# Optimization experiments

Hardware: AMD Instinct MI355X
Metric: run time of the kernel (lower is better)

## Reference

```python
import jax, jax.numpy as jnp
import numpy as np

TOP_K = 2
NUM_EXPERTS = 64


def setup_inputs() -> dict:
    key = jax.random.key(0)
    k1, k2 = jax.random.split(key)
    bs, sq, h = 4, 4096, 4096
    x = jax.random.normal(k1, (bs, sq, h), dtype=jnp.float32)
    expert_mask = jnp.ones((bs, NUM_EXPERTS), dtype=jnp.float32)
    # router weight: torch.nn.Linear(hidden, num_experts, bias=False) -> [E, H]
    W = jax.random.normal(k2, (NUM_EXPERTS, h), dtype=jnp.float32) * 0.02
    return {"x": x, "expert_mask": expert_mask, "W": W}


def reference(x, expert_mask, W):
    bs, sq, h = x.shape
    # logits = Linear(x.view(-1, h)) : [bs*sq, E]
    logits = jnp.einsum("bsh,eh->bse", x, W).reshape(bs * sq, NUM_EXPERTS)
    scores = jax.nn.softmax(logits, axis=-1)
    # expert_mask [bs, E] broadcast over seq
    scores = (expert_mask[:, None, :] * scores.reshape(bs, sq, NUM_EXPERTS)).reshape(
        bs * sq, NUM_EXPERTS
    )
    expert_weights, expert_indices = jax.lax.top_k(scores, TOP_K)  # [bs*sq, k]
    expert_weights = jax.nn.softmax(expert_weights, axis=-1)
    # moe_normalize_expert_weights = 1 -> L1 norm renormalization
    expert_weights = expert_weights / jnp.sum(
        jnp.abs(expert_weights), axis=-1, keepdims=True
    )
    return scores, logits, expert_weights, expert_indices
```

## Files before the change

kernel.cpp:

```cpp
#include <hip/hip_runtime.h>
#include <hip/hip_bf16.h>

#define NE     64
#define HDIM   4096
#define NTOK   16384
#define KSPLIT 8
#define KPER   (HDIM / KSPLIT)
#define KC     32
#define NT     (KPER / KC)
#define NCHUNK (HDIM / 32)
#define TOKB   128
#define PT     130

typedef __attribute__((ext_vector_type(8))) short bf16x8;
typedef __attribute__((ext_vector_type(4))) float f32x4;

union FragU { uint4 u; bf16x8 v; };

__device__ __forceinline__ unsigned rne_bf16(float f) {
    unsigned v = __float_as_uint(f);
    return (v + 0x7FFFu + ((v >> 16) & 1u)) >> 16;
}

__device__ __forceinline__ void split8f(const float* s, FragU& hi, FragU& lo) {
#pragma unroll
    for (int w = 0; w < 4; ++w) {
        const unsigned u0 = __float_as_uint(s[2 * w]);
        const unsigned u1 = __float_as_uint(s[2 * w + 1]);
        const unsigned h0 = u0 & 0xFFFF0000u, h1 = u1 & 0xFFFF0000u;
        ((unsigned*)&hi.u)[w] = (h0 >> 16) | h1;
        const float l0 = __uint_as_float(u0) - __uint_as_float(h0);
        const float l1 = __uint_as_float(u1) - __uint_as_float(h1);
        ((unsigned*)&lo.u)[w] = rne_bf16(l0) | (rne_bf16(l1) << 16);
    }
}

__global__ __launch_bounds__(256) void prep_w(
    const float* __restrict__ W, uint4* __restrict__ wfh, uint4* __restrict__ wfl) {
    const int idx = blockIdx.x * 256 + threadIdx.x;
    const int l  = idx & 63;
    const int ce = idx >> 6;
    const int e  = ce & 3;
    const int c  = ce >> 2;
    const float* src = W + (size_t)(e * 16 + (l & 15)) * HDIM + c * 32 + (l >> 4) * 8;

    unsigned hw[4], lw[4];
#pragma unroll
    for (int w = 0; w < 4; ++w) {
        const float x0 = src[2 * w], x1 = src[2 * w + 1];
        const unsigned u0 = __float_as_uint(x0), u1 = __float_as_uint(x1);
        const unsigned h0 = u0 & 0xFFFF0000u, h1 = u1 & 0xFFFF0000u;
        hw[w] = (h0 >> 16) | h1;
        const float l0 = x0 - __uint_as_float(h0);
        const float l1 = x1 - __uint_as_float(h1);
        lw[w] = rne_bf16(l0) | (rne_bf16(l1) << 16);
    }
    wfh[idx] = make_uint4(hw[0], hw[1], hw[2], hw[3]);
    wfl[idx] = make_uint4(lw[0], lw[1], lw[2], lw[3]);
}

#define MFMA_STEP(AH0, AL0, AH1, AL1, WH, WL)                                          \
    _Pragma("unroll")                                                                   \
    for (int e = 0; e < 4; ++e) {                                                       \
        acc[0][e] = __builtin_amdgcn_mfma_f32_16x16x32_bf16(AH0.v, WH[e].v, acc[0][e], 0, 0, 0); \
        acc[0][e] = __builtin_amdgcn_mfma_f32_16x16x32_bf16(AL0.v, WH[e].v, acc[0][e], 0, 0, 0); \
        acc[0][e] = __builtin_amdgcn_mfma_f32_16x16x32_bf16(AH0.v, WL[e].v, acc[0][e], 0, 0, 0); \
        acc[1][e] = __builtin_amdgcn_mfma_f32_16x16x32_bf16(AH1.v, WH[e].v, acc[1][e], 0, 0, 0); \
        acc[1][e] = __builtin_amdgcn_mfma_f32_16x16x32_bf16(AL1.v, WH[e].v, acc[1][e], 0, 0, 0); \
        acc[1][e] = __builtin_amdgcn_mfma_f32_16x16x32_bf16(AH1.v, WL[e].v, acc[1][e], 0, 0, 0); \
    }

__global__ __launch_bounds__(256) void gemm_logits_mfma(
    const float* __restrict__ x, const uint4* __restrict__ wfh,
    const uint4* __restrict__ wfl, float* __restrict__ part0,
    float* __restrict__ wspart) {
    __shared__ float xs[2][KC][PT];

    const int tid  = threadIdx.x;
    const int lane = tid & 63;
    const int wv   = tid >> 6;
    const int t0   = blockIdx.x * TOKB;
    const int bk   = blockIdx.y;
    const int r    = lane & 15;
    const int u    = lane >> 4;

    f32x4 acc[2][4];
#pragma unroll
    for (int f = 0; f < 2; ++f)
#pragma unroll
        for (int e = 0; e < 4; ++e) acc[f][e] = (f32x4){0.f, 0.f, 0.f, 0.f};

    const int srow = tid >> 3;
    const int skq  = tid & 7;
    const float* gsrc = x + (size_t)(t0 + srow) * HDIM + bk * KPER + skq * 4;

    const uint4* whb = wfh + (size_t)(bk * NT) * 256 + lane;
    const uint4* wlb = wfl + (size_t)(bk * NT) * 256 + lane;

    float4 ldE[4], ldO[4];
    FragU WhA[4], WlA[4], WhB[4], WlB[4];

#define LOADT(LD, T)                                                              \
    _Pragma("unroll")                                                             \
    for (int p = 0; p < 4; ++p)                                                   \
        LD[p] = *reinterpret_cast<const float4*>(gsrc + (size_t)(32 * p) * HDIM + (T) * KC);

#define WRITET(B, LD)                                                             \
    _Pragma("unroll")                                                             \
    for (int p = 0; p < 4; ++p) {                                                 \
        const int rr = srow + 32 * p;                                             \
        xs[B][skq * 4 + 0][rr] = LD[p].x;                                         \
        xs[B][skq * 4 + 1][rr] = LD[p].y;                                         \
        xs[B][skq * 4 + 2][rr] = LD[p].z;                                         \
        xs[B][skq * 4 + 3][rr] = LD[p].w;                                         \
    }

#define COMPUTE(B, WH, WL_)                                                       \
    {                                                                             \
        float a0[8], a1[8];                                                       \
        const float* xb = &xs[B][0][0] + (u * 8) * PT + crow;                     \
        _Pragma("unroll")                                                         \
        for (int j = 0; j < 8; ++j) { a0[j] = xb[j * PT]; a1[j] = xb[j * PT + 16]; } \
        FragU ah0, al0, ah1, al1;                                                 \
        split8f(a0, ah0, al0);                                                    \
        split8f(a1, ah1, al1);                                                    \
        MFMA_STEP(ah0, al0, ah1, al1, WH, WL_)                                    \
    }

    const int crow = wv * 32 + r;

#pragma unroll
    for (int e = 0; e < 4; ++e) { WhA[e].u = whb[e * 64]; WlA[e].u = wlb[e * 64]; }
    LOADT(ldE, 0)
    LOADT(ldO, 1)
    WRITET(0, ldE)
    LOADT(ldE, 2)
    __syncthreads();

    for (int t2 = 0; t2 < NT; t2 += 2) {
        {
            const size_t c = (size_t)(t2 + 1) * 256;
#pragma unroll
            for (int e = 0; e < 4; ++e) { WhB[e].u = whb[c + e * 64]; WlB[e].u = wlb[c + e * 64]; }
            WRITET(1, ldO)
            if (t2 + 3 < NT) { LOADT(ldO, t2 + 3) }
            COMPUTE(0, WhA, WlA)
            __syncthreads();
        }
        {
            const int tn = t2 + 2;
            if (tn < NT) {
                const size_t c = (size_t)tn * 256;
#pragma unroll
                for (int e = 0; e < 4; ++e) { WhA[e].u = whb[c + e * 64]; WlA[e].u = wlb[c + e * 64]; }
                WRITET(0, ldE)
                if (t2 + 4 < NT) { LOADT(ldE, t2 + 4) }
            }
            COMPUTE(1, WhB, WlB)
            if (tn < NT) { __syncthreads(); }
        }
    }

    float* dst = (bk == 0 ? part0 : wspart + (size_t)(bk - 1) * NTOK * NE);
#pragma unroll
    for (int f = 0; f < 2; ++f)
#pragma unroll
        for (int e = 0; e < 4; ++e)
#pragma unroll
            for (int rr = 0; rr < 4; ++rr)
                dst[(size_t)(t0 + wv * 32 + f * 16 + u * 4 + rr) * NE + e * 16 + r] = acc[f][e][rr];
#undef LOADT
#undef WRITET
#undef COMPUTE
}

__global__ __launch_bounds__(256) void router_kernel(
    const float* __restrict__ wspart, const float* __restrict__ mask,
    float* __restrict__ out, int ksplit) {
    const int lane = threadIdx.x & 63;
    const int wv   = threadIdx.x >> 6;
    const int t    = blockIdx.x * 4 + wv;

    float* lo = out + (size_t)NTOK * NE + (size_t)t * NE;
    float l = lo[lane];
    for (int c = 1; c < ksplit; ++c)
        l += wspart[((size_t)(c - 1) * NTOK + t) * NE + lane];
    lo[lane] = l;

    float mx = l;
#pragma unroll
    for (int m = 32; m; m >>= 1) mx = fmaxf(mx, __shfl_xor(mx, m, 64));
    const float ev = __expf(l - mx);
    float s = ev;
#pragma unroll
    for (int m = 32; m; m >>= 1) s += __shfl_xor(s, m, 64);
    const float sc = mask[(size_t)(t >> 12) * NE + lane] * (ev / s);
    out[(size_t)t * NE + lane] = sc;

    const unsigned long long key =
        ((unsigned long long)__float_as_uint(sc) << 6) | (unsigned long long)(63 - lane);
    unsigned long long k1 = key;
#pragma unroll
    for (int m = 32; m; m >>= 1) {
        const unsigned long long o = __shfl_xor(k1, m, 64);
        if (o > k1) k1 = o;
    }
    const int   i1 = 63 - (int)(k1 & 63ull);
    const float v1 = __uint_as_float((unsigned)(k1 >> 6));

    unsigned long long k2 = (lane == i1) ? 0ull : key;
#pragma unroll
    for (int m = 32; m; m >>= 1) {
        const unsigned long long o = __shfl_xor(k2, m, 64);
        if (o > k2) k2 = o;
    }
    const int   i2 = 63 - (int)(k2 & 63ull);
    const float v2 = __uint_as_float((unsigned)(k2 >> 6));

    if (lane == 0) {
        const float e2v = __expf(v2 - v1);
        float w1 = 1.f / (1.f + e2v);
        float w2 = e2v / (1.f + e2v);
        const float sw = w1 + w2;
        w1 /= sw; w2 /= sw;
        const size_t wo = (size_t)2 * NTOK * NE;
        out[wo + (size_t)t * 2 + 0] = w1;
        out[wo + (size_t)t * 2 + 1] = w2;
        const size_t io = wo + (size_t)NTOK * 2;
        out[io + (size_t)t * 2 + 0] = (float)i1;
        out[io + (size_t)t * 2 + 1] = (float)i2;
    }
}

extern "C" void kernel_launch(void* const* d_in, const int* in_sizes, int n_in,
                              void* d_out, int out_size, void* d_ws, size_t ws_size,
                              hipStream_t stream) {
    const float* x    = (const float*)d_in[0];
    const float* mask = (const float*)d_in[1];
    const float* W    = (const float*)d_in[2];
    float* out = (float*)d_out;
    float* ws  = (float*)d_ws;

    float* wspart = ws;
    uint4* wfh = (uint4*)(ws + (size_t)(KSPLIT - 1) * NTOK * NE);
    uint4* wfl = wfh + (size_t)NCHUNK * 4 * 64;
    float* part0 = out + (size_t)NTOK * NE;

    prep_w<<<dim3(NCHUNK * 4 * 64 / 256), dim3(256), 0, stream>>>(W, wfh, wfl);
    gemm_logits_mfma<<<dim3(NTOK / TOKB, KSPLIT), dim3(256), 0, stream>>>(
        x, wfh, wfl, part0, wspart);
    router_kernel<<<dim3(NTOK / 4), dim3(256), 0, stream>>>(wspart, mask, out, KSPLIT);
}
```

Before: 83.80 us.

## Replace grid K-split with in-block wave K-split and shared-memory reduction

Removes the cross-block split-K over hidden dimension that wrote seven partial logit slabs to global workspace, which the router kernel then re-read and summed. Each block now covers 32 tokens over the full hidden dimension, with its four waves splitting K inside the block. The partial sums are reduced in shared memory and written once as final logits. This cuts global partial-sum traffic and the router's extra reads, but each block now runs a longer K loop, the grid is 512 one-dimensional blocks, and W fragments are reused across fewer tokens per load.

```diff
diff --git a/kernel.cpp b/kernel.cpp
--- a/kernel.cpp
+++ b/kernel.cpp
@@ -4,13 +4,12 @@
 #define NE     64
 #define HDIM   4096
 #define NTOK   16384
-#define KSPLIT 8
-#define KPER   (HDIM / KSPLIT)
-#define KC     32
-#define NT     (KPER / KC)
+#define TOKB   32
+#define KPH    128
+#define NPH    (HDIM / KPH)
 #define NCHUNK (HDIM / 32)
-#define TOKB   128
-#define PT     130
+#define PT     33
+#define RST    65
 
 typedef __attribute__((ext_vector_type(8))) short bf16x8;
 typedef __attribute__((ext_vector_type(4))) float f32x4;
@@ -72,17 +71,16 @@
 
 __global__ __launch_bounds__(256) void gemm_logits_mfma(
     const float* __restrict__ x, const uint4* __restrict__ wfh,
-    const uint4* __restrict__ wfl, float* __restrict__ part0,
-    float* __restrict__ wspart) {
-    __shared__ float xs[2][KC][PT];
+    const uint4* __restrict__ wfl, float* __restrict__ logits) {
+    __shared__ float xs[2][KPH][PT];
 
     const int tid  = threadIdx.x;
     const int lane = tid & 63;
     const int wv   = tid >> 6;
     const int t0   = blockIdx.x * TOKB;
-    const int bk   = blockIdx.y;
     const int r    = lane & 15;
     const int u    = lane >> 4;
+    const int wk   = wv * 32;
 
     f32x4 acc[2][4];
 #pragma unroll
@@ -90,12 +88,12 @@
 #pragma unroll
         for (int e = 0; e < 4; ++e) acc[f][e] = (f32x4){0.f, 0.f, 0.f, 0.f};
 
-    const int srow = tid >> 3;
-    const int skq  = tid & 7;
-    const float* gsrc = x + (size_t)(t0 + srow) * HDIM + bk * KPER + skq * 4;
-
-    const uint4* whb = wfh + (size_t)(bk * NT) * 256 + lane;
-    const uint4* wlb = wfl + (size_t)(bk * NT) * 256 + lane;
+    const int trow = tid >> 3;
+    const int kq   = tid & 7;
+    const float* gsrc = x + (size_t)(t0 + trow) * HDIM + kq * 4;
+
+    const uint4* whb = wfh + lane;
+    const uint4* wlb = wfl + lane;
 
     float4 ldE[4], ldO[4];
     FragU WhA[4], WlA[4], WhB[4], WlB[4];
@@ -103,22 +101,31 @@
 #define LOADT(LD, T)                                                              \
     _Pragma("unroll")                                                             \
     for (int p = 0; p < 4; ++p)                                                   \
-        LD[p] = *reinterpret_cast<const float4*>(gsrc + (size_t)(32 * p) * HDIM + (T) * KC);
+        LD[p] = *reinterpret_cast<const float4*>(gsrc + (T) * KPH + p * 32);
 
 #define WRITET(B, LD)                                                             \
     _Pragma("unroll")                                                             \
     for (int p = 0; p < 4; ++p) {                                                 \
-        const int rr = srow + 32 * p;                                             \
-        xs[B][skq * 4 + 0][rr] = LD[p].x;                                         \
-        xs[B][skq * 4 + 1][rr] = LD[p].y;                                         \
-        xs[B][skq * 4 + 2][rr] = LD[p].z;                                         \
-        xs[B][skq * 4 + 3][rr] = LD[p].w;                                         \
+        xs[B][kq * 4 + p * 32 + 0][trow] = LD[p].x;                               \
+        xs[B][kq * 4 + p * 32 + 1][trow] = LD[p].y;                               \
+        xs[B][kq * 4 + p * 32 + 2][trow] = LD[p].z;                               \
+        xs[B][kq * 4 + p * 32 + 3][trow] = LD[p].w;                               \
+    }
+
+#define LOADW(WH, WL_, CC)                                                        \
+    {                                                                             \
+        const size_t c_ = (size_t)(CC) * 256;                                     \
+        _Pragma("unroll")                                                         \
+        for (int e = 0; e < 4; ++e) {                                             \
+            WH[e].u = whb[c_ + e * 64];                                           \
+            WL_[e].u = wlb[c_ + e * 64];                                          \
+        }                                                                         \
     }
 
 #define COMPUTE(B, WH, WL_)                                                       \
     {                                                                             \
         float a0[8], a1[8];                                                       \
-        const float* xb = &xs[B][0][0] + (u * 8) * PT + crow;                     \
+        const float* xb = &xs[B][wk + u * 8][0] + r;                              \
         _Pragma("unroll")                                                         \
         for (int j = 0; j < 8; ++j) { a0[j] = xb[j * PT]; a1[j] = xb[j * PT + 16]; } \
         FragU ah0, al0, ah1, al1;                                                 \
@@ -127,65 +134,72 @@
         MFMA_STEP(ah0, al0, ah1, al1, WH, WL_)                                    \
     }
 
-    const int crow = wv * 32 + r;
-
-#pragma unroll
-    for (int e = 0; e < 4; ++e) { WhA[e].u = whb[e * 64]; WlA[e].u = wlb[e * 64]; }
+    LOADW(WhA, WlA, wv)
     LOADT(ldE, 0)
     LOADT(ldO, 1)
     WRITET(0, ldE)
     LOADT(ldE, 2)
     __syncthreads();
 
-    for (int t2 = 0; t2 < NT; t2 += 2) {
+    for (int t2 = 0; t2 < NPH; t2 += 2) {
         {
-            const size_t c = (size_t)(t2 + 1) * 256;
-#pragma unroll
-            for (int e = 0; e < 4; ++e) { WhB[e].u = whb[c + e * 64]; WlB[e].u = wlb[c + e * 64]; }
+            LOADW(WhB, WlB, 4 * (t2 + 1) + wv)
+            COMPUTE(0, WhA, WlA)
             WRITET(1, ldO)
-            if (t2 + 3 < NT) { LOADT(ldO, t2 + 3) }
-            COMPUTE(0, WhA, WlA)
+            if (t2 + 3 < NPH) { LOADT(ldO, t2 + 3) }
             __syncthreads();
         }
         {
             const int tn = t2 + 2;
-            if (tn < NT) {
-                const size_t c = (size_t)tn * 256;
-#pragma unroll
-                for (int e = 0; e < 4; ++e) { WhA[e].u = whb[c + e * 64]; WlA[e].u = wlb[c + e * 64]; }
+            if (tn < NPH) { LOADW(WhA, WlA, 4 * tn + wv) }
+            COMPUTE(1, WhB, WlB)
+            if (tn < NPH) {
                 WRITET(0, ldE)
-                if (t2 + 4 < NT) { LOADT(ldE, t2 + 4) }
+                if (t2 + 4 < NPH) { LOADT(ldE, t2 + 4) }
+                __syncthreads();
             }
-            COMPUTE(1, WhB, WlB)
-            if (tn < NT) { __syncthreads(); }
         }
     }
 
-    float* dst = (bk == 0 ? part0 : wspart + (size_t)(bk - 1) * NTOK * NE);
+    float* red = &xs[0][0][0];
+    __syncthreads();
 #pragma unroll
     for (int f = 0; f < 2; ++f)
 #pragma unroll
         for (int e = 0; e < 4; ++e)
 #pragma unroll
             for (int rr = 0; rr < 4; ++rr)
-                dst[(size_t)(t0 + wv * 32 + f * 16 + u * 4 + rr) * NE + e * 16 + r] = acc[f][e][rr];
+                red[wv * (TOKB * RST) + (f * 16 + u * 4 + rr) * RST + e * 16 + r] =
+                    acc[f][e][rr];
+    __syncthreads();
+
+    const int stok = tid >> 3;
+    const int se0  = (tid & 7) * 8;
+    float sum[8];
+#pragma unroll
+    for (int i = 0; i < 8; ++i) {
+        float s = red[stok * RST + se0 + i];
+#pragma unroll
+        for (int w = 1; w < 4; ++w)
+            s += red[w * (TOKB * RST) + stok * RST + se0 + i];
+        sum[i] = s;
+    }
+    float* lrow = logits + (size_t)(t0 + stok) * NE + se0;
+    *reinterpret_cast<float4*>(lrow)     = make_float4(sum[0], sum[1], sum[2], sum[3]);
+    *reinterpret_cast<float4*>(lrow + 4) = make_float4(sum[4], sum[5], sum[6], sum[7]);
 #undef LOADT
 #undef WRITET
+#undef LOADW
 #undef COMPUTE
 }
 
 __global__ __launch_bounds__(256) void router_kernel(
-    const float* __restrict__ wspart, const float* __restrict__ mask,
-    float* __restrict__ out, int ksplit) {
+    const float* __restrict__ mask, float* __restrict__ out) {
     const int lane = threadIdx.x & 63;
     const int wv   = threadIdx.x >> 6;
     const int t    = blockIdx.x * 4 + wv;
 
-    float* lo = out + (size_t)NTOK * NE + (size_t)t * NE;
-    float l = lo[lane];
-    for (int c = 1; c < ksplit; ++c)
-        l += wspart[((size_t)(c - 1) * NTOK + t) * NE + lane];
-    lo[lane] = l;
+    const float l = out[(size_t)NTOK * NE + (size_t)t * NE + lane];
 
     float mx = l;
 #pragma unroll
@@ -239,15 +253,13 @@
     const float* mask = (const float*)d_in[1];
     const float* W    = (const float*)d_in[2];
     float* out = (float*)d_out;
-    float* ws  = (float*)d_ws;
-
-    float* wspart = ws;
-    uint4* wfh = (uint4*)(ws + (size_t)(KSPLIT - 1) * NTOK * NE);
+
+    uint4* wfh = (uint4*)d_ws;
     uint4* wfl = wfh + (size_t)NCHUNK * 4 * 64;
-    float* part0 = out + (size_t)NTOK * NE;
+    float* logits = out + (size_t)NTOK * NE;
 
     prep_w<<<dim3(NCHUNK * 4 * 64 / 256), dim3(256), 0, stream>>>(W, wfh, wfl);
-    gemm_logits_mfma<<<dim3(NTOK / TOKB, KSPLIT), dim3(256), 0, stream>>>(
-        x, wfh, wfl, part0, wspart);
-    router_kernel<<<dim3(NTOK / 4), dim3(256), 0, stream>>>(wspart, mask, out, KSPLIT);
-}
+    gemm_logits_mfma<<<dim3(NTOK / TOKB), dim3(256), 0, stream>>>(
+        x, wfh, wfl, logits);
+    router_kernel<<<dim3(NTOK / 4), dim3(256), 0, stream>>>(mask, out);
+}
```

Result: faster. 81.51 us (-2.7%).
